# Kernel tuning notes

Measured on AMD Instinct MI355X. Metric: run time of the kernel, lower is better.

The kernel has to match this reference:

```python
import jax, jax.numpy as jnp
import numpy as np

NA, NPAPER, IN, HID, H, D, OUT, E = 16384, 16384, 128, 64, 4, 16, 349, 262144
NEG_SLOPE = 0.2  # DGL GATConv default leaky_relu slope


def _gat(hs, hd, src, dst, W, al, ar, b, n_dst):
    # DGL GATConv: shared fc, additive attention, edge softmax per dst, weighted sum.
    fs = (hs @ W).reshape(-1, H, D)            # [Ns,H,D]
    fd = (hd @ W).reshape(-1, H, D)            # [Nd,H,D]
    el = jnp.sum(fs * al, axis=-1)             # [Ns,H]
    er = jnp.sum(fd * ar, axis=-1)             # [Nd,H]
    e = jax.nn.leaky_relu(el[src] + er[dst], NEG_SLOPE)  # [E,H]
    m = jax.ops.segment_max(e, dst, num_segments=n_dst)
    m = jnp.where(jnp.isfinite(m), m, 0.0)
    ex = jnp.exp(e - m[dst])
    den = jax.ops.segment_sum(ex, dst, num_segments=n_dst)
    alpha = ex / jnp.maximum(den[dst], 1e-9)   # [E,H]
    out = jax.ops.segment_sum(fs[src] * alpha[..., None], dst, num_segments=n_dst)
    return out + b.reshape(1, H, D)


def _ln(x, g, b):
    m = jnp.mean(x, -1, keepdims=True)
    v = jnp.mean((x - m) ** 2, -1, keepdims=True)
    return (x - m) / jnp.sqrt(v + 1e-5) * g + b


def setup_inputs() -> dict:
    key = jax.random.key(0)
    ks = jax.random.split(key, 30)
    def n(k, shp, s=1.0):
        return jax.random.normal(ks[k], shp, jnp.float32) * s
    def ridx(k, hi):
        return jax.random.randint(ks[k], (E,), 0, hi)
    return dict(
        x_author=n(0, (NA, IN)), x_paper=n(1, (NPAPER, IN)),
        ntype_emb=n(2, (2, IN), 0.5),
        W0=n(3, (3, IN, HID), 0.1), al0=n(4, (3, H, D), 0.1), ar0=n(5, (3, H, D), 0.1), b0=jnp.zeros((3, HID), jnp.float32),
        W1=n(6, (3, HID, HID), 0.1), al1=n(7, (3, H, D), 0.1), ar1=n(8, (3, H, D), 0.1), b1=jnp.zeros((3, HID), jnp.float32),
        ln1_gb=jnp.array([1.0, 0.0], jnp.float32),
        attn_w=n(9, (4,), 0.5), attn_b=n(10, (4,), 0.1),
        ln2_gb=jnp.array([1.0, 0.0], jnp.float32),
        ffn_w1=n(11, (1, 16), 0.5), ffn_b1=jnp.zeros((16,), jnp.float32),
        ffn_w2=n(12, (16, 1), 0.5), ffn_b2=jnp.zeros((1,), jnp.float32),
        lin_W=n(13, (2 * HID, OUT), 0.1), lin_b=jnp.zeros((OUT,), jnp.float32),
        src_writes=ridx(14, NA), dst_writes=ridx(15, NPAPER),
        src_cites=ridx(16, NPAPER), dst_cites=ridx(17, NPAPER),
        src_revw=ridx(18, NPAPER), dst_revw=ridx(19, NA),
    )


def reference(x_author, x_paper, ntype_emb, W0, al0, ar0, b0, W1, al1, ar1, b1,
              ln1_gb, attn_w, attn_b, ln2_gb, ffn_w1, ffn_b1, ffn_w2, ffn_b2,
              lin_W, lin_b,
              src_writes, dst_writes, src_cites, dst_cites, src_revw, dst_revw):
    # node-type embedding scaling (x[nty] * ntype_emb[i])
    ha = x_author * ntype_emb[0]
    hp = x_paper * ntype_emb[1]

    def hetero(ha, hp, W, al, ar, b):
        # HeteroGraphConv with sum aggregation over etypes per dst ntype
        op = _gat(ha, hp, src_writes, dst_writes, W[0], al[0], ar[0], b[0], NPAPER) \
           + _gat(hp, hp, src_cites, dst_cites, W[1], al[1], ar[1], b[1], NPAPER)
        oa = _gat(hp, ha, src_revw, dst_revw, W[2], al[2], ar[2], b[2], NA)
        return oa.reshape(NA, HID), op.reshape(NPAPER, HID)

    ha, hp = hetero(ha, hp, W0, al0, ar0, b0)
    ha, hp = jax.nn.relu(ha), jax.nn.relu(hp)  # dropout = identity at eval
    ha, hp = hetero(ha, hp, W1, al1, ar1, b1)

    h1 = hp                                   # [NP, HID]
    x = h1[:, :, None]                        # [NP, HID, 1]: feature dims as tokens, d=1
    # DALayer (pre-LN transformer encoder layer, 1 head, d=1, scale=1)
    y = _ln(x, ln1_gb[0], ln1_gb[1])
    q = y * attn_w[0] + attn_b[0]
    k = y * attn_w[1] + attn_b[1]
    v = y * attn_w[2] + attn_b[2]
    att = jax.nn.softmax(jnp.einsum('nsd,ntd->nst', q, k), axis=-1)  # [NP,HID,HID]
    o = jnp.einsum('nst,ntd->nsd', att, v) * attn_w[3] + attn_b[3]
    x = x + o
    y = _ln(x, ln2_gb[0], ln2_gb[1])
    f = jax.nn.gelu(y @ ffn_w1 + ffn_b1, approximate=False) @ ffn_w2 + ffn_b2
    x = x + f
    h2 = x[:, :, 0]                           # squeeze

    def l2n(z):
        return z / jnp.maximum(jnp.linalg.norm(z, axis=1, keepdims=True), 1e-12)

    hf = jnp.concatenate([l2n(h1), l2n(h2)], axis=1)  # [NP, 2*HID]
    return hf @ lin_W + lin_b
```

## Files before the change

kernel.cpp:

```cpp
#include <hip/hip_runtime.h>
#include <math.h>

constexpr int N_A   = 16384;
constexpr int N_P   = 16384;
constexpr int IN_D  = 128;
constexpr int HID   = 64;
constexpr int NH    = 4;
constexpr int OUTD  = 349;
constexpr int NE    = 262144;
constexpr int NB    = 64;
constexpr float NEG = 0.2f;

__device__ __forceinline__ float lrelu(float x) { return x > 0.f ? x : NEG * x; }

__global__ __launch_bounds__(256) void k_chist(const int* __restrict__ dW, const int* __restrict__ dC,
                                               const int* __restrict__ dR, int* __restrict__ ccnt) {
    __shared__ int h[256];
    const int t = blockIdx.y;
    const int* __restrict__ d = t == 0 ? dW : t == 1 ? dC : dR;
    const int tid = threadIdx.x;
    h[tid] = 0;
    __syncthreads();
    const int base = blockIdx.x * 4096;
#pragma unroll
    for (int i = 0; i < 16; ++i) {
        int dst = d[base + i * 256 + tid];
        atomicAdd(&h[dst >> 6], 1);
    }
    __syncthreads();
    ccnt[(t * NB + blockIdx.x) * 256 + tid] = h[tid];
}

__global__ __launch_bounds__(768) void k_coffs(const int* __restrict__ ccnt, int* __restrict__ coffs,
                                               int* __restrict__ crow) {
    const int tid = threadIdx.x;
    const int t = tid >> 8, bin = tid & 255;
    int total = 0;
    for (int b = 0; b < NB; ++b) total += ccnt[(t * NB + b) * 256 + bin];
    __shared__ int sc[768];
    sc[tid] = total;
    __syncthreads();
    for (int w = 1; w < 256; w <<= 1) {
        int v = (bin >= w) ? sc[tid - w] : 0;
        __syncthreads();
        sc[tid] += v;
        __syncthreads();
    }
    const int incl = sc[tid];
    const int base = incl - total;
    crow[t * 257 + bin] = base;
    if (bin == 255) crow[t * 257 + 256] = incl;
    int run = base;
    for (int b = 0; b < NB; ++b) {
        int c = ccnt[(t * NB + b) * 256 + bin];
        coffs[(t * NB + b) * 256 + bin] = run;
        run += c;
    }
}

__global__ __launch_bounds__(256) void k_cscatter(const int* __restrict__ sW, const int* __restrict__ dW,
                                                  const int* __restrict__ sC, const int* __restrict__ dC,
                                                  const int* __restrict__ sR, const int* __restrict__ dR,
                                                  const int* __restrict__ coffs,
                                                  int* __restrict__ ebW, int* __restrict__ ebC,
                                                  int* __restrict__ ebR) {
    __shared__ int cur[256];
    const int t = blockIdx.y;
    const int* __restrict__ sp = t == 0 ? sW : t == 1 ? sC : sR;
    const int* __restrict__ dp = t == 0 ? dW : t == 1 ? dC : dR;
    int* __restrict__ eb = t == 0 ? ebW : t == 1 ? ebC : ebR;
    const int tid = threadIdx.x;
    cur[tid] = coffs[(t * NB + blockIdx.x) * 256 + tid];
    __syncthreads();
    const int base = blockIdx.x * 4096;
#pragma unroll
    for (int i = 0; i < 16; ++i) {
        int e = base + i * 256 + tid;
        int dst = dp[e], src = sp[e];
        int pos = atomicAdd(&cur[dst >> 6], 1);
        eb[pos] = src | ((dst & 63) << 14);
    }
}

__global__ __launch_bounds__(256) void k_fine(const int* __restrict__ crow,
                                              const int* __restrict__ ebW, const int* __restrict__ ebC,
                                              const int* __restrict__ ebR,
                                              int* __restrict__ row,
                                              int* __restrict__ esW, int* __restrict__ esC,
                                              int* __restrict__ esR) {
    __shared__ int bins[64], exc[64], cur[64];
    const int t = blockIdx.y, cb = blockIdx.x, tid = threadIdx.x;
    const int* __restrict__ eb = t == 0 ? ebW : t == 1 ? ebC : ebR;
    int* __restrict__ es = t == 0 ? esW : t == 1 ? esC : esR;
    const int lo = crow[t * 257 + cb], hi = crow[t * 257 + cb + 1];
    if (tid < 64) bins[tid] = 0;
    __syncthreads();
    for (int e = lo + tid; e < hi; e += 256) atomicAdd(&bins[eb[e] >> 14], 1);
    __syncthreads();
    if (tid == 0) {
        int r = 0;
#pragma unroll
        for (int j = 0; j < 64; ++j) { exc[j] = r; cur[j] = r; r += bins[j]; }
    }
    __syncthreads();
    if (tid < 64) row[t * 16385 + cb * 64 + tid] = lo + exc[tid];
    if (tid == 0 && cb == 255) row[t * 16385 + 16384] = crow[t * 257 + 256];
    for (int e = lo + tid; e < hi; e += 256) {
        int v = eb[e];
        int pos = atomicAdd(&cur[v >> 14], 1);
        es[lo + pos] = v & 16383;
    }
}

struct GemmJobs {
    const float* X[5];  const float* W[5];  const float* NT[5];
    float* F[5];        float* EL[5];       float* ER[5];
    const float* AL[5]; const float* AR[5];
};

template <int K, int RELU>
__global__ __launch_bounds__(256) void k_gemm(GemmJobs j) {
    __shared__ float Wc[32 * 64];
    __shared__ float XT[32][68];

    const float* __restrict__ X;  const float* __restrict__ Wp;  const float* __restrict__ NTp;
    float* __restrict__ F;  float* __restrict__ EL;  float* __restrict__ ER;
    const float* __restrict__ AL; const float* __restrict__ AR;
    switch (blockIdx.z) {
      case 0: X=j.X[0]; Wp=j.W[0]; NTp=j.NT[0]; F=j.F[0]; EL=j.EL[0]; ER=j.ER[0]; AL=j.AL[0]; AR=j.AR[0]; break;
      case 1: X=j.X[1]; Wp=j.W[1]; NTp=j.NT[1]; F=j.F[1]; EL=j.EL[1]; ER=j.ER[1]; AL=j.AL[1]; AR=j.AR[1]; break;
      case 2: X=j.X[2]; Wp=j.W[2]; NTp=j.NT[2]; F=j.F[2]; EL=j.EL[2]; ER=j.ER[2]; AL=j.AL[2]; AR=j.AR[2]; break;
      case 3: X=j.X[3]; Wp=j.W[3]; NTp=j.NT[3]; F=j.F[3]; EL=j.EL[3]; ER=j.ER[3]; AL=j.AL[3]; AR=j.AR[3]; break;
      default: X=j.X[4]; Wp=j.W[4]; NTp=j.NT[4]; F=j.F[4]; EL=j.EL[4]; ER=j.ER[4]; AL=j.AL[4]; AR=j.AR[4]; break;
    }

    const int tid = threadIdx.x;
    const int tx  = tid & 15;
    const int rg  = tid >> 4;
    const int r0  = blockIdx.x * 64;

    float acc[4][4] = {};

    for (int kc = 0; kc < K; kc += 32) {
        __syncthreads();
#pragma unroll
        for (int it = 0; it < 2; ++it) {
            int idx = tid * 4 + it * 1024;
            int k = idx >> 6, c = idx & 63;
            *(float4*)(Wc + idx) = *(const float4*)(Wp + (size_t)(kc + k) * 64 + c);
        }
#pragma unroll
        for (int it = 0; it < 2; ++it) {
            int idx = tid * 4 + it * 1024;
            int row = idx >> 5, col = idx & 31;
            float4 v = *(const float4*)(X + (size_t)(r0 + row) * K + kc + col);
            if (RELU) {
                v.x = fmaxf(v.x, 0.f); v.y = fmaxf(v.y, 0.f);
                v.z = fmaxf(v.z, 0.f); v.w = fmaxf(v.w, 0.f);
            }
            if (NTp) {
                float4 s = *(const float4*)(NTp + kc + col);
                v.x *= s.x; v.y *= s.y; v.z *= s.z; v.w *= s.w;
            }
            XT[col + 0][row] = v.x;
            XT[col + 1][row] = v.y;
            XT[col + 2][row] = v.z;
            XT[col + 3][row] = v.w;
        }
        __syncthreads();
#pragma unroll
        for (int kk = 0; kk < 32; ++kk) {
            float4 a4 = *(const float4*)(&XT[kk][rg * 4]);
            float4 w4 = *(const float4*)(Wc + kk * 64 + tx * 4);
            acc[0][0] = fmaf(a4.x, w4.x, acc[0][0]); acc[0][1] = fmaf(a4.x, w4.y, acc[0][1]);
            acc[0][2] = fmaf(a4.x, w4.z, acc[0][2]); acc[0][3] = fmaf(a4.x, w4.w, acc[0][3]);
            acc[1][0] = fmaf(a4.y, w4.x, acc[1][0]); acc[1][1] = fmaf(a4.y, w4.y, acc[1][1]);
            acc[1][2] = fmaf(a4.y, w4.z, acc[1][2]); acc[1][3] = fmaf(a4.y, w4.w, acc[1][3]);
            acc[2][0] = fmaf(a4.z, w4.x, acc[2][0]); acc[2][1] = fmaf(a4.z, w4.y, acc[2][1]);
            acc[2][2] = fmaf(a4.z, w4.z, acc[2][2]); acc[2][3] = fmaf(a4.z, w4.w, acc[2][3]);
            acc[3][0] = fmaf(a4.w, w4.x, acc[3][0]); acc[3][1] = fmaf(a4.w, w4.y, acc[3][1]);
            acc[3][2] = fmaf(a4.w, w4.z, acc[3][2]); acc[3][3] = fmaf(a4.w, w4.w, acc[3][3]);
        }
    }

    if (F) {
#pragma unroll
        for (int i = 0; i < 4; ++i) {
            size_t n = (size_t)r0 + rg * 4 + i;
            *(float4*)(F + n * 64 + tx * 4) =
                make_float4(acc[i][0], acc[i][1], acc[i][2], acc[i][3]);
        }
    }
    if (EL) {
        float4 alv = ((const float4*)AL)[tx];
#pragma unroll
        for (int i = 0; i < 4; ++i) {
            float p = acc[i][0] * alv.x + acc[i][1] * alv.y +
                      acc[i][2] * alv.z + acc[i][3] * alv.w;
            p += __shfl_xor(p, 1, 64);
            p += __shfl_xor(p, 2, 64);
            if ((tx & 3) == 0) EL[((size_t)r0 + rg * 4 + i) * 4 + (tx >> 2)] = p;
        }
    }
    if (ER) {
        float4 arv = ((const float4*)AR)[tx];
#pragma unroll
        for (int i = 0; i < 4; ++i) {
            float p = acc[i][0] * arv.x + acc[i][1] * arv.y +
                      acc[i][2] * arv.z + acc[i][3] * arv.w;
            p += __shfl_xor(p, 1, 64);
            p += __shfl_xor(p, 2, 64);
            if ((tx & 3) == 0) ER[((size_t)r0 + rg * 4 + i) * 4 + (tx >> 2)] = p;
        }
    }
}

struct AggType { const int* row; const int* es; const float* el; const float* er; const float* fs; };
struct AggArgs { AggType t[3]; const float* b; float* op; float* oa; };

__device__ __forceinline__ float4 agg16v(const int* __restrict__ rowv, const int* __restrict__ es,
                                         const float* __restrict__ el, const float* __restrict__ er,
                                         const float* __restrict__ fs, int d, int lane,
                                         float* denOut) {
    float4 acc = make_float4(0.f, 0.f, 0.f, 0.f);
    float den = 0.f;
    int start = rowv[d], deg = rowv[d + 1] - start;
    if (deg > 0) {
        const int j16 = lane & 15;
        const int g   = lane >> 4;
        const int h   = j16 >> 2;
        const float rh = er[(size_t)d * 4 + g];
        for (int e0 = 0; e0 < deg; e0 += 16) {
            int o = e0 + j16;
            int sn = es[start + (o < deg ? o : 0)];
            float wv = 0.f;
            if (o < deg) wv = __expf(lrelu(el[(size_t)sn * 4 + g] + rh));
            den += wv;
#pragma unroll
            for (int sub = 0; sub < 4; ++sub) {
                int eidx = sub * 4 + g;
                int snj  = __shfl(sn, eidx, 64);
                float wj = __shfl(wv, (h << 4) + eidx, 64);
                float4 f4 = *(const float4*)(fs + (size_t)snj * 64 + j16 * 4);
                acc.x = fmaf(wj, f4.x, acc.x);
                acc.y = fmaf(wj, f4.y, acc.y);
                acc.z = fmaf(wj, f4.z, acc.z);
                acc.w = fmaf(wj, f4.w, acc.w);
            }
        }
    }
    *denOut = den;
    return acc;
}

__device__ __forceinline__ float4 agg_finish(float4 acc, float den, int lane) {
#pragma unroll
    for (int w = 1; w < 16; w <<= 1) den += __shfl_xor(den, w, 64);
#pragma unroll
    for (int w = 16; w < 64; w <<= 1) {
        acc.x += __shfl_xor(acc.x, w, 64);
        acc.y += __shfl_xor(acc.y, w, 64);
        acc.z += __shfl_xor(acc.z, w, 64);
        acc.w += __shfl_xor(acc.w, w, 64);
    }
    float denh = __shfl(den, (((lane & 15) >> 2) << 4), 64);
    float inv = 1.f / fmaxf(denh, 1e-9f);
    acc.x *= inv; acc.y *= inv; acc.z *= inv; acc.w *= inv;
    return acc;
}

__global__ __launch_bounds__(256) void k_agg(AggArgs A) {
    int wid = (blockIdx.x * 256 + threadIdx.x) >> 6;
    int lane = threadIdx.x & 63;
    int c16 = lane & 15;
    if (wid < N_P) {
        float d0, d1;
        float4 a0 = agg16v(A.t[0].row, A.t[0].es, A.t[0].el, A.t[0].er, A.t[0].fs, wid, lane, &d0);
        float4 a1 = agg16v(A.t[1].row, A.t[1].es, A.t[1].el, A.t[1].er, A.t[1].fs, wid, lane, &d1);
        a0 = agg_finish(a0, d0, lane);
        a1 = agg_finish(a1, d1, lane);
        if (lane < 16) {
            float4 b0 = *(const float4*)(A.b + c16 * 4);
            float4 b1 = *(const float4*)(A.b + 64 + c16 * 4);
            float4 o = make_float4(a0.x + a1.x + b0.x + b1.x,
                                   a0.y + a1.y + b0.y + b1.y,
                                   a0.z + a1.z + b0.z + b1.z,
                                   a0.w + a1.w + b0.w + b1.w);
            *(float4*)(A.op + (size_t)wid * 64 + c16 * 4) = o;
        }
    } else {
        int d = wid - N_P;
        float d2;
        float4 a2 = agg16v(A.t[2].row, A.t[2].es, A.t[2].el, A.t[2].er, A.t[2].fs, d, lane, &d2);
        a2 = agg_finish(a2, d2, lane);
        if (lane < 16) {
            float4 b2 = *(const float4*)(A.b + 128 + c16 * 4);
            float4 o = make_float4(a2.x + b2.x, a2.y + b2.y, a2.z + b2.z, a2.w + b2.w);
            *(float4*)(A.oa + (size_t)d * 64 + c16 * 4) = o;
        }
    }
}

__global__ __launch_bounds__(256) void k_hf(const float* __restrict__ h1, float* __restrict__ hf,
                                            const float* __restrict__ ln1gb,
                                            const float* __restrict__ aw, const float* __restrict__ ab,
                                            const float* __restrict__ ln2gb,
                                            const float* __restrict__ fw1, const float* __restrict__ fb1,
                                            const float* __restrict__ fw2, const float* __restrict__ fb2) {
    __shared__ float Cs;
    if (threadIdx.x == 0) {
        float y1 = ln1gb[1];
        float v  = y1 * aw[2] + ab[2];
        float o  = v * aw[3] + ab[3];
        float y2 = ln2gb[1];
        float f  = fb2[0];
#pragma unroll
        for (int q = 0; q < 16; ++q) {
            float zz = y2 * fw1[q] + fb1[q];
            f += 0.5f * zz * (1.f + erff(zz * 0.70710678118654752f)) * fw2[q];
        }
        Cs = o + f;
    }
    __syncthreads();
    float C = Cs;
    int lane = threadIdx.x & 63;
    int row  = blockIdx.x * 4 + (threadIdx.x >> 6);
    float v1 = h1[(size_t)row * 64 + lane];
    float s1 = v1 * v1;
#pragma unroll
    for (int w = 1; w < 64; w <<= 1) s1 += __shfl_xor(s1, w, 64);
    float o1 = v1 / fmaxf(sqrtf(s1), 1e-12f);
    float v2 = v1 + C;
    float s2 = v2 * v2;
#pragma unroll
    for (int w = 1; w < 64; w <<= 1) s2 += __shfl_xor(s2, w, 64);
    float o2 = v2 / fmaxf(sqrtf(s2), 1e-12f);
    hf[(size_t)row * 128 + lane]      = o1;
    hf[(size_t)row * 128 + 64 + lane] = o2;
}

__global__ __launch_bounds__(256) void k_gemm_out(const float* __restrict__ X,
                                                  const float* __restrict__ W,
                                                  const float* __restrict__ bias,
                                                  float* __restrict__ out) {
    __shared__ float Wc[32 * 64];
    __shared__ float XT[32][68];
    const int tid = threadIdx.x;
    const int tx  = tid & 15;
    const int rg  = tid >> 4;
    const int r0  = blockIdx.x * 64;
    const int c0  = blockIdx.y * 64;

    float acc[4][4] = {};

    for (int kc = 0; kc < 128; kc += 32) {
        __syncthreads();
#pragma unroll
        for (int it = 0; it < 2; ++it) {
            int idx = tid * 4 + it * 1024;
            int k = idx >> 6, c = idx & 63;
            int gk = kc + k;
            float4 v;
            int gc = c0 + c;
            v.x = (gc + 0 < OUTD) ? W[(size_t)gk * OUTD + gc + 0] : 0.f;
            v.y = (gc + 1 < OUTD) ? W[(size_t)gk * OUTD + gc + 1] : 0.f;
            v.z = (gc + 2 < OUTD) ? W[(size_t)gk * OUTD + gc + 2] : 0.f;
            v.w = (gc + 3 < OUTD) ? W[(size_t)gk * OUTD + gc + 3] : 0.f;
            *(float4*)(Wc + idx) = v;
        }
#pragma unroll
        for (int it = 0; it < 2; ++it) {
            int idx = tid * 4 + it * 1024;
            int row = idx >> 5, col = idx & 31;
            float4 v = *(const float4*)(X + (size_t)(r0 + row) * 128 + kc + col);
            XT[col + 0][row] = v.x;
            XT[col + 1][row] = v.y;
            XT[col + 2][row] = v.z;
            XT[col + 3][row] = v.w;
        }
        __syncthreads();
#pragma unroll
        for (int kk = 0; kk < 32; ++kk) {
            float4 a4 = *(const float4*)(&XT[kk][rg * 4]);
            float4 w4 = *(const float4*)(Wc + kk * 64 + tx * 4);
            acc[0][0] = fmaf(a4.x, w4.x, acc[0][0]); acc[0][1] = fmaf(a4.x, w4.y, acc[0][1]);
            acc[0][2] = fmaf(a4.x, w4.z, acc[0][2]); acc[0][3] = fmaf(a4.x, w4.w, acc[0][3]);
            acc[1][0] = fmaf(a4.y, w4.x, acc[1][0]); acc[1][1] = fmaf(a4.y, w4.y, acc[1][1]);
            acc[1][2] = fmaf(a4.y, w4.z, acc[1][2]); acc[1][3] = fmaf(a4.y, w4.w, acc[1][3]);
            acc[2][0] = fmaf(a4.z, w4.x, acc[2][0]); acc[2][1] = fmaf(a4.z, w4.y, acc[2][1]);
            acc[2][2] = fmaf(a4.z, w4.z, acc[2][2]); acc[2][3] = fmaf(a4.z, w4.w, acc[2][3]);
            acc[3][0] = fmaf(a4.w, w4.x, acc[3][0]); acc[3][1] = fmaf(a4.w, w4.y, acc[3][1]);
            acc[3][2] = fmaf(a4.w, w4.z, acc[3][2]); acc[3][3] = fmaf(a4.w, w4.w, acc[3][3]);
        }
    }

    float b4[4];
#pragma unroll
    for (int q = 0; q < 4; ++q) {
        int c = c0 + tx * 4 + q;
        b4[q] = (c < OUTD) ? bias[c] : 0.f;
    }
#pragma unroll
    for (int i = 0; i < 4; ++i) {
        size_t n = (size_t)r0 + rg * 4 + i;
#pragma unroll
        for (int q = 0; q < 4; ++q) {
            int c = c0 + tx * 4 + q;
            if (c < OUTD) out[n * OUTD + c] = acc[i][q] + b4[q];
        }
    }
}

extern "C" void kernel_launch(void* const* d_in, const int* in_sizes, int n_in,
                              void* d_out, int out_size, void* d_ws, size_t ws_size,
                              hipStream_t stream) {
    const float* x_author = (const float*)d_in[0];
    const float* x_paper  = (const float*)d_in[1];
    const float* ntype    = (const float*)d_in[2];
    const float* W0  = (const float*)d_in[3];
    const float* al0 = (const float*)d_in[4];
    const float* ar0 = (const float*)d_in[5];
    const float* b0  = (const float*)d_in[6];
    const float* W1  = (const float*)d_in[7];
    const float* al1 = (const float*)d_in[8];
    const float* ar1 = (const float*)d_in[9];
    const float* b1  = (const float*)d_in[10];
    const float* ln1gb = (const float*)d_in[11];
    const float* attw  = (const float*)d_in[12];
    const float* attb  = (const float*)d_in[13];
    const float* ln2gb = (const float*)d_in[14];
    const float* fw1 = (const float*)d_in[15];
    const float* fb1 = (const float*)d_in[16];
    const float* fw2 = (const float*)d_in[17];
    const float* fb2 = (const float*)d_in[18];
    const float* linW = (const float*)d_in[19];
    const float* linb = (const float*)d_in[20];
    const int* srcW = (const int*)d_in[21];
    const int* dstW = (const int*)d_in[22];
    const int* srcC = (const int*)d_in[23];
    const int* dstC = (const int*)d_in[24];
    const int* srcR = (const int*)d_in[25];
    const int* dstR = (const int*)d_in[26];
    float* out = (float*)d_out;

    float* ws = (float*)d_ws;
    size_t off = 0;
    float* fsW = ws + off; off += (size_t)N_A * HID;
    float* fsC = ws + off; off += (size_t)N_P * HID;
    float* fsR = ws + off; off += (size_t)N_P * HID;
    float* elw = ws + off; off += (size_t)N_A * NH;
    float* erw = ws + off; off += (size_t)N_P * NH;
    float* elc = ws + off; off += (size_t)N_P * NH;
    float* erc = ws + off; off += (size_t)N_P * NH;
    float* elr = ws + off; off += (size_t)N_P * NH;
    float* err = ws + off; off += (size_t)N_A * NH;
    float* oa0 = ws + off; off += (size_t)N_A * HID;
    float* op0 = ws + off; off += (size_t)N_P * HID;
    float* oa1 = ws + off; off += (size_t)N_A * HID;
    float* op1 = ws + off; off += (size_t)N_P * HID;
    float* hf  = ws + off; off += (size_t)N_P * 2 * HID;
    int* ccnt  = (int*)(ws + off); off += 3 * NB * 256;
    int* coffs = (int*)(ws + off); off += 3 * NB * 256;
    int* crow  = (int*)(ws + off); off += 3 * 257 + 1;
    int* row   = (int*)(ws + off); off += 3 * 16385 + 1;
    int* ebW  = (int*)(ws + off); off += NE;
    int* ebC  = (int*)(ws + off); off += NE;
    int* ebR  = (int*)(ws + off); off += NE;
    int* esW  = (int*)(ws + off); off += NE;
    int* esC  = (int*)(ws + off); off += NE;
    int* esR  = (int*)(ws + off); off += NE;

    const int* rowW = row;
    const int* rowC = row + 16385;
    const int* rowR = row + 2 * 16385;

    const float* ntA = ntype;
    const float* ntP = ntype + IN_D;

    GemmJobs j0{};
    j0.X[0] = x_author; j0.W[0] = W0;                  j0.NT[0] = ntA;
    j0.F[0] = fsW; j0.EL[0] = elw; j0.ER[0] = nullptr; j0.AL[0] = al0;       j0.AR[0] = nullptr;
    j0.X[1] = x_paper;  j0.W[1] = W0;                  j0.NT[1] = ntP;
    j0.F[1] = nullptr; j0.EL[1] = nullptr; j0.ER[1] = erw; j0.AL[1] = nullptr; j0.AR[1] = ar0;
    j0.X[2] = x_paper;  j0.W[2] = W0 + IN_D * HID;     j0.NT[2] = ntP;
    j0.F[2] = fsC; j0.EL[2] = elc; j0.ER[2] = erc;     j0.AL[2] = al0 + 64;  j0.AR[2] = ar0 + 64;
    j0.X[3] = x_paper;  j0.W[3] = W0 + 2 * IN_D * HID; j0.NT[3] = ntP;
    j0.F[3] = fsR; j0.EL[3] = elr; j0.ER[3] = nullptr; j0.AL[3] = al0 + 128; j0.AR[3] = nullptr;
    j0.X[4] = x_author; j0.W[4] = W0 + 2 * IN_D * HID; j0.NT[4] = ntA;
    j0.F[4] = nullptr; j0.EL[4] = nullptr; j0.ER[4] = err; j0.AL[4] = nullptr; j0.AR[4] = ar0 + 128;

    GemmJobs j1{};
    j1.X[0] = oa0; j1.W[0] = W1;                   j1.NT[0] = nullptr;
    j1.F[0] = fsW; j1.EL[0] = elw; j1.ER[0] = nullptr; j1.AL[0] = al1;       j1.AR[0] = nullptr;
    j1.X[1] = op0; j1.W[1] = W1;                   j1.NT[1] = nullptr;
    j1.F[1] = nullptr; j1.EL[1] = nullptr; j1.ER[1] = erw; j1.AL[1] = nullptr; j1.AR[1] = ar1;
    j1.X[2] = op0; j1.W[2] = W1 + HID * HID;       j1.NT[2] = nullptr;
    j1.F[2] = fsC; j1.EL[2] = elc; j1.ER[2] = erc;     j1.AL[2] = al1 + 64;  j1.AR[2] = ar1 + 64;
    j1.X[3] = op0; j1.W[3] = W1 + 2 * HID * HID;   j1.NT[3] = nullptr;
    j1.F[3] = fsR; j1.EL[3] = elr; j1.ER[3] = nullptr; j1.AL[3] = al1 + 128; j1.AR[3] = nullptr;
    j1.X[4] = oa0; j1.W[4] = W1 + 2 * HID * HID;   j1.NT[4] = nullptr;
    j1.F[4] = nullptr; j1.EL[4] = nullptr; j1.ER[4] = err; j1.AL[4] = nullptr; j1.AR[4] = ar1 + 128;

    AggArgs a0{};
    a0.t[0] = {rowW, esW, elw, erw, fsW};
    a0.t[1] = {rowC, esC, elc, erc, fsC};
    a0.t[2] = {rowR, esR, elr, err, fsR};
    a0.b = b0; a0.op = op0; a0.oa = oa0;
    AggArgs a1 = a0;
    a1.b = b1; a1.op = op1; a1.oa = oa1;

    k_chist<<<dim3(NB, 3), 256, 0, stream>>>(dstW, dstC, dstR, ccnt);
    k_coffs<<<1, 768, 0, stream>>>(ccnt, coffs, crow);
    k_cscatter<<<dim3(NB, 3), 256, 0, stream>>>(srcW, dstW, srcC, dstC, srcR, dstR,
                                                coffs, ebW, ebC, ebR);
    k_fine<<<dim3(256, 3), 256, 0, stream>>>(crow, ebW, ebC, ebR, row, esW, esC, esR);

    k_gemm<IN_D, 0><<<dim3(N_A / 64, 1, 5), 256, 0, stream>>>(j0);
    k_agg<<<(N_P + N_A) / 4, 256, 0, stream>>>(a0);

    k_gemm<HID, 1><<<dim3(N_A / 64, 1, 5), 256, 0, stream>>>(j1);
    k_agg<<<(N_P + N_A) / 4, 256, 0, stream>>>(a1);

    k_hf<<<N_P / 4, 256, 0, stream>>>(op1, hf, ln1gb, attw, attb, ln2gb, fw1, fb1, fw2, fb2);
    k_gemm_out<<<dim3(N_P / 64, (OUTD + 63) / 64), 256, 0, stream>>>(hf, linW, linb, out);
}
```

Before: 160.1 us.

## Skip dead author branch in last GAT layer and fuse hf normalization into aggregation

The final layer's author output is never used, so the second GEMM launches only three jobs and the second aggregation processes paper nodes only. The paper aggregation now also computes the constant DALayer offset and both L2 normalizations, writing hf directly. This removes the separate k_hf kernel and the op1/oa1 round trip through global memory. In exchange, every warp recomputes the constant, including 16 erff evaluations.

```diff
diff --git a/kernel.cpp b/kernel.cpp
--- a/kernel.cpp
+++ b/kernel.cpp
@@ -216,7 +216,12 @@
 }
 
 struct AggType { const int* row; const int* es; const float* el; const float* er; const float* fs; };
-struct AggArgs { AggType t[3]; const float* b; float* op; float* oa; };
+struct AggArgs {
+    AggType t[3]; const float* b; float* op; float* oa;
+    float* hf;
+    const float* ln1gb; const float* aw; const float* ab; const float* ln2gb;
+    const float* fw1; const float* fb1; const float* fw2; const float* fb2;
+};
 
 __device__ __forceinline__ float4 agg16v(const int* __restrict__ rowv, const int* __restrict__ es,
                                          const float* __restrict__ el, const float* __restrict__ er,
@@ -269,74 +274,78 @@
     return acc;
 }
 
+template <int L1>
 __global__ __launch_bounds__(256) void k_agg(AggArgs A) {
     int wid = (blockIdx.x * 256 + threadIdx.x) >> 6;
     int lane = threadIdx.x & 63;
     int c16 = lane & 15;
-    if (wid < N_P) {
+    if (L1 == 0) {
+        if (wid < N_P) {
+            float d0, d1;
+            float4 a0 = agg16v(A.t[0].row, A.t[0].es, A.t[0].el, A.t[0].er, A.t[0].fs, wid, lane, &d0);
+            float4 a1 = agg16v(A.t[1].row, A.t[1].es, A.t[1].el, A.t[1].er, A.t[1].fs, wid, lane, &d1);
+            a0 = agg_finish(a0, d0, lane);
+            a1 = agg_finish(a1, d1, lane);
+            if (lane < 16) {
+                float4 b0 = *(const float4*)(A.b + c16 * 4);
+                float4 b1 = *(const float4*)(A.b + 64 + c16 * 4);
+                float4 o = make_float4(a0.x + a1.x + b0.x + b1.x,
+                                       a0.y + a1.y + b0.y + b1.y,
+                                       a0.z + a1.z + b0.z + b1.z,
+                                       a0.w + a1.w + b0.w + b1.w);
+                *(float4*)(A.op + (size_t)wid * 64 + c16 * 4) = o;
+            }
+        } else {
+            int d = wid - N_P;
+            float d2;
+            float4 a2 = agg16v(A.t[2].row, A.t[2].es, A.t[2].el, A.t[2].er, A.t[2].fs, d, lane, &d2);
+            a2 = agg_finish(a2, d2, lane);
+            if (lane < 16) {
+                float4 b2 = *(const float4*)(A.b + 128 + c16 * 4);
+                float4 o = make_float4(a2.x + b2.x, a2.y + b2.y, a2.z + b2.z, a2.w + b2.w);
+                *(float4*)(A.oa + (size_t)d * 64 + c16 * 4) = o;
+            }
+        }
+    } else {
         float d0, d1;
         float4 a0 = agg16v(A.t[0].row, A.t[0].es, A.t[0].el, A.t[0].er, A.t[0].fs, wid, lane, &d0);
         float4 a1 = agg16v(A.t[1].row, A.t[1].es, A.t[1].el, A.t[1].er, A.t[1].fs, wid, lane, &d1);
         a0 = agg_finish(a0, d0, lane);
         a1 = agg_finish(a1, d1, lane);
+        float4 b0 = *(const float4*)(A.b + c16 * 4);
+        float4 b1 = *(const float4*)(A.b + 64 + c16 * 4);
+        float4 o = make_float4(a0.x + a1.x + b0.x + b1.x,
+                               a0.y + a1.y + b0.y + b1.y,
+                               a0.z + a1.z + b0.z + b1.z,
+                               a0.w + a1.w + b0.w + b1.w);
+        float y1 = A.ln1gb[1];
+        float vv = y1 * A.aw[2] + A.ab[2];
+        float oo = vv * A.aw[3] + A.ab[3];
+        float y2 = A.ln2gb[1];
+        float f  = A.fb2[0];
+#pragma unroll
+        for (int q = 0; q < 16; ++q) {
+            float zz = y2 * A.fw1[q] + A.fb1[q];
+            f += 0.5f * zz * (1.f + erff(zz * 0.70710678118654752f)) * A.fw2[q];
+        }
+        float C = oo + f;
+        float4 oc = make_float4(o.x + C, o.y + C, o.z + C, o.w + C);
+        float s1 = o.x * o.x + o.y * o.y + o.z * o.z + o.w * o.w;
+        float s2 = oc.x * oc.x + oc.y * oc.y + oc.z * oc.z + oc.w * oc.w;
+#pragma unroll
+        for (int w = 1; w < 16; w <<= 1) {
+            s1 += __shfl_xor(s1, w, 64);
+            s2 += __shfl_xor(s2, w, 64);
+        }
+        float i1 = 1.f / fmaxf(sqrtf(s1), 1e-12f);
+        float i2 = 1.f / fmaxf(sqrtf(s2), 1e-12f);
         if (lane < 16) {
-            float4 b0 = *(const float4*)(A.b + c16 * 4);
-            float4 b1 = *(const float4*)(A.b + 64 + c16 * 4);
-            float4 o = make_float4(a0.x + a1.x + b0.x + b1.x,
-                                   a0.y + a1.y + b0.y + b1.y,
-                                   a0.z + a1.z + b0.z + b1.z,
-                                   a0.w + a1.w + b0.w + b1.w);
-            *(float4*)(A.op + (size_t)wid * 64 + c16 * 4) = o;
-        }
-    } else {
-        int d = wid - N_P;
-        float d2;
-        float4 a2 = agg16v(A.t[2].row, A.t[2].es, A.t[2].el, A.t[2].er, A.t[2].fs, d, lane, &d2);
-        a2 = agg_finish(a2, d2, lane);
-        if (lane < 16) {
-            float4 b2 = *(const float4*)(A.b + 128 + c16 * 4);
-            float4 o = make_float4(a2.x + b2.x, a2.y + b2.y, a2.z + b2.z, a2.w + b2.w);
-            *(float4*)(A.oa + (size_t)d * 64 + c16 * 4) = o;
-        }
-    }
-}
-
-__global__ __launch_bounds__(256) void k_hf(const float* __restrict__ h1, float* __restrict__ hf,
-                                            const float* __restrict__ ln1gb,
-                                            const float* __restrict__ aw, const float* __restrict__ ab,
-                                            const float* __restrict__ ln2gb,
-                                            const float* __restrict__ fw1, const float* __restrict__ fb1,
-                                            const float* __restrict__ fw2, const float* __restrict__ fb2) {
-    __shared__ float Cs;
-    if (threadIdx.x == 0) {
-        float y1 = ln1gb[1];
-        float v  = y1 * aw[2] + ab[2];
-        float o  = v * aw[3] + ab[3];
-        float y2 = ln2gb[1];
-        float f  = fb2[0];
-#pragma unroll
-        for (int q = 0; q < 16; ++q) {
-            float zz = y2 * fw1[q] + fb1[q];
-            f += 0.5f * zz * (1.f + erff(zz * 0.70710678118654752f)) * fw2[q];
-        }
-        Cs = o + f;
-    }
-    __syncthreads();
-    float C = Cs;
-    int lane = threadIdx.x & 63;
-    int row  = blockIdx.x * 4 + (threadIdx.x >> 6);
-    float v1 = h1[(size_t)row * 64 + lane];
-    float s1 = v1 * v1;
-#pragma unroll
-    for (int w = 1; w < 64; w <<= 1) s1 += __shfl_xor(s1, w, 64);
-    float o1 = v1 / fmaxf(sqrtf(s1), 1e-12f);
-    float v2 = v1 + C;
-    float s2 = v2 * v2;
-#pragma unroll
-    for (int w = 1; w < 64; w <<= 1) s2 += __shfl_xor(s2, w, 64);
-    float o2 = v2 / fmaxf(sqrtf(s2), 1e-12f);
-    hf[(size_t)row * 128 + lane]      = o1;
-    hf[(size_t)row * 128 + 64 + lane] = o2;
+            *(float4*)(A.hf + (size_t)wid * 128 + c16 * 4) =
+                make_float4(o.x * i1, o.y * i1, o.z * i1, o.w * i1);
+            *(float4*)(A.hf + (size_t)wid * 128 + 64 + c16 * 4) =
+                make_float4(oc.x * i2, oc.y * i2, oc.z * i2, oc.w * i2);
+        }
+    }
 }
 
 __global__ __launch_bounds__(256) void k_gemm_out(const float* __restrict__ X,
@@ -456,8 +465,6 @@
     float* err = ws + off; off += (size_t)N_A * NH;
     float* oa0 = ws + off; off += (size_t)N_A * HID;
     float* op0 = ws + off; off += (size_t)N_P * HID;
-    float* oa1 = ws + off; off += (size_t)N_A * HID;
-    float* op1 = ws + off; off += (size_t)N_P * HID;
     float* hf  = ws + off; off += (size_t)N_P * 2 * HID;
     int* ccnt  = (int*)(ws + off); off += 3 * NB * 256;
     int* coffs = (int*)(ws + off); off += 3 * NB * 256;
@@ -496,10 +503,6 @@
     j1.F[1] = nullptr; j1.EL[1] = nullptr; j1.ER[1] = erw; j1.AL[1] = nullptr; j1.AR[1] = ar1;
     j1.X[2] = op0; j1.W[2] = W1 + HID * HID;       j1.NT[2] = nullptr;
     j1.F[2] = fsC; j1.EL[2] = elc; j1.ER[2] = erc;     j1.AL[2] = al1 + 64;  j1.AR[2] = ar1 + 64;
-    j1.X[3] = op0; j1.W[3] = W1 + 2 * HID * HID;   j1.NT[3] = nullptr;
-    j1.F[3] = fsR; j1.EL[3] = elr; j1.ER[3] = nullptr; j1.AL[3] = al1 + 128; j1.AR[3] = nullptr;
-    j1.X[4] = oa0; j1.W[4] = W1 + 2 * HID * HID;   j1.NT[4] = nullptr;
-    j1.F[4] = nullptr; j1.EL[4] = nullptr; j1.ER[4] = err; j1.AL[4] = nullptr; j1.AR[4] = ar1 + 128;
 
     AggArgs a0{};
     a0.t[0] = {rowW, esW, elw, erw, fsW};
@@ -507,7 +510,10 @@
     a0.t[2] = {rowR, esR, elr, err, fsR};
     a0.b = b0; a0.op = op0; a0.oa = oa0;
     AggArgs a1 = a0;
-    a1.b = b1; a1.op = op1; a1.oa = oa1;
+    a1.b = b1; a1.op = nullptr; a1.oa = nullptr;
+    a1.hf = hf;
+    a1.ln1gb = ln1gb; a1.aw = attw; a1.ab = attb; a1.ln2gb = ln2gb;
+    a1.fw1 = fw1; a1.fb1 = fb1; a1.fw2 = fw2; a1.fb2 = fb2;
 
     k_chist<<<dim3(NB, 3), 256, 0, stream>>>(dstW, dstC, dstR, ccnt);
     k_coffs<<<1, 768, 0, stream>>>(ccnt, coffs, crow);
@@ -516,11 +522,10 @@
     k_fine<<<dim3(256, 3), 256, 0, stream>>>(crow, ebW, ebC, ebR, row, esW, esC, esR);
 
     k_gemm<IN_D, 0><<<dim3(N_A / 64, 1, 5), 256, 0, stream>>>(j0);
-    k_agg<<<(N_P + N_A) / 4, 256, 0, stream>>>(a0);
-
-    k_gemm<HID, 1><<<dim3(N_A / 64, 1, 5), 256, 0, stream>>>(j1);
-    k_agg<<<(N_P + N_A) / 4, 256, 0, stream>>>(a1);
-
-    k_hf<<<N_P / 4, 256, 0, stream>>>(op1, hf, ln1gb, attw, attb, ln2gb, fw1, fb1, fw2, fb2);
+    k_agg<0><<<(N_P + N_A) / 4, 256, 0, stream>>>(a0);
+
+    k_gemm<HID, 1><<<dim3(N_A / 64, 1, 3), 256, 0, stream>>>(j1);
+    k_agg<1><<<N_P / 4, 256, 0, stream>>>(a1);
+
     k_gemm_out<<<dim3(N_P / 64, (OUTD + 63) / 64), 256, 0, stream>>>(hf, linW, linb, out);
 }
```

Measured after the change: 148.9 us, median of 2. -7.0%, faster.
